# Optimization experiments

Hardware: AMD Instinct MI355X
Metric: run time of the kernel (lower is better)

## Reference

```python
import jax, jax.numpy as jnp
import numpy as np

E = 128   # embed_dim / node feature width
H = 4     # num_heads
B = 512   # number of graphs
N = 65536 # total nodes


def setup_inputs() -> dict:
    key = jax.random.key(0)
    ks = jax.random.split(key, 12)
    s = 1.0 / np.sqrt(E)
    batch = jnp.sort(jax.random.randint(ks[0], (N,), 0, B))
    return {
        "x": jax.random.normal(ks[1], (N, E), jnp.float32),
        "metal_x": jax.random.normal(ks[2], (B, E), jnp.float32),
        "batch": batch,
        "Wk": jax.random.normal(ks[3], (E, E), jnp.float32) * s,
        "bk": jnp.zeros((E,), jnp.float32),
        "Wq": jax.random.normal(ks[4], (E, E), jnp.float32) * s,
        "bq": jnp.zeros((E,), jnp.float32),
        "in_w": jax.random.normal(ks[5], (3 * E, E), jnp.float32) * s,
        "in_b": jnp.zeros((3 * E,), jnp.float32),
        "out_w": jax.random.normal(ks[6], (E, E), jnp.float32) * s,
        "out_b": jnp.zeros((E,), jnp.float32),
    }


def reference(x, metal_x, batch, Wk, bk, Wq, bq, in_w, in_b, out_w, out_b):
    n, e = x.shape
    b = metal_x.shape[0]
    nb = np.asarray(batch)
    counts_np = np.bincount(nb, minlength=b)            # nodes per graph
    L = int(counts_np.max()) + 1                        # +1 for metal token at pos 0
    counts = jnp.asarray(counts_np)
    offsets = jnp.asarray(np.concatenate([[0], np.cumsum(counts_np)[:-1]]))
    pos = jnp.arange(n) - offsets[batch] + 1            # within-graph slot (metal at 0)

    # pad_sequence: value [L, B, E], slot 0 = metal_x, slots 1.. = graph nodes
    value = jnp.zeros((L, b, e), x.dtype)
    value = value.at[pos, batch].set(x)
    value = value.at[0, jnp.arange(b)].set(metal_x)

    # FCNN key/query (single hidden linear + relu, no output head)
    k_in = jax.nn.relu(value @ Wk.T + bk)
    q_in = jax.nn.relu(value @ Wq.T + bq)

    # MultiheadAttention (batch_first=False): in_proj then per-head scaled dot-product
    hd = e // H
    q = (q_in @ in_w[:e].T + in_b[:e]).reshape(L, b, H, hd)
    k = (k_in @ in_w[e:2 * e].T + in_b[e:2 * e]).reshape(L, b, H, hd)
    v = (value @ in_w[2 * e:].T + in_b[2 * e:]).reshape(L, b, H, hd)

    scores = jnp.einsum("lbhd,mbhd->bhlm", q, k) * (hd ** -0.5)
    valid = jnp.arange(L)[None, :] < (counts + 1)[:, None]   # [B, L] key_padding mask
    scores = jnp.where(valid[:, None, None, :], scores, jnp.finfo(scores.dtype).min)
    attn = jax.nn.softmax(scores, axis=-1)
    ctx = jnp.einsum("bhlm,mbhd->lbhd", attn, v).reshape(L, b, e)
    out = ctx @ out_w.T + out_b

    x_out = out[pos, batch]      # packed node outputs [N, E]
    metal_out = out[0]           # metal token outputs [B, E]
    return x_out, metal_out
```

## Files before the change

kernel.cpp:

```cpp
#include <hip/hip_runtime.h>

#define E   128
#define HD  32
#define NB  512
#define NN  65536
#define TT  (NB + NN)
#define TE  ((size_t)TT * 128)

typedef __attribute__((ext_vector_type(8))) short short8;
typedef __attribute__((ext_vector_type(4))) float f32x4;

__device__ __forceinline__ const float* row_ptr(const float* base, const float* metal, int t) {
  return (t < NB) ? metal + (size_t)t * E : base + (size_t)(t - NB) * E;
}
__device__ __forceinline__ float* row_ptr_w(float* base, float* metal, int t) {
  return (t < NB) ? metal + (size_t)t * E : base + (size_t)(t - NB) * E;
}

__device__ __forceinline__ unsigned short f2bf_rne(float x) {
  unsigned u = __float_as_uint(x);
  return (unsigned short)((u + 0x7FFFu + ((u >> 16) & 1u)) >> 16);
}
__device__ __forceinline__ void split_bf(float x, unsigned short& h, unsigned short& l) {
  h = f2bf_rne(x);
  float hf = __uint_as_float(((unsigned)h) << 16);
  l = f2bf_rne(x - hf);
}

__global__ void k_setup(const int* __restrict__ batch, int* __restrict__ start,
                        const float* __restrict__ Wq, const float* __restrict__ Wk,
                        const float* __restrict__ in_w, const float* __restrict__ out_w,
                        unsigned short* __restrict__ Wh, unsigned short* __restrict__ Wl) {
  int b = blockIdx.x;
  if (b < 256) {
    int i = b * 256 + threadIdx.x;
    int bi = batch[i];
    int bp = (i == 0) ? -1 : batch[i - 1];
    for (int g = bp + 1; g <= bi; ++g) start[g] = i;
    if (i == NN - 1)
      for (int g = bi + 1; g <= NB; ++g) start[g] = NN;
  } else {
    int idx = (b - 256) * 256 + threadIdx.x;
    int r = idx >> 7, c = idx & 127;
    float v;
    if (r < 128)      v = Wq[r * 128 + c];
    else if (r < 256) v = Wk[(r - 128) * 128 + c];
    else if (r < 640) v = in_w[(r - 256) * 128 + c];
    else              v = out_w[(r - 640) * 128 + c];
    unsigned short h, l;
    split_bf(v, h, l);
    Wh[idx] = h;
    Wl[idx] = l;
  }
}

__global__ void k_seqmap(const int* __restrict__ batch, const int* __restrict__ start,
                         int* __restrict__ seqmap) {
  int t = blockIdx.x * 256 + threadIdx.x;
  if (t >= TT) return;
  seqmap[t] = (t < NB) ? (start[t] + t) : (t - NB + batch[t - NB] + 1);
}

__global__ __launch_bounds__(256, 2)
void k_outproj(const unsigned short* __restrict__ Ch, const unsigned short* __restrict__ Cl,
               const int* __restrict__ rowmap,
               const unsigned short* __restrict__ Wh, const unsigned short* __restrict__ Wl,
               const float* __restrict__ bias,
               float* __restrict__ Cx, float* __restrict__ Cm) {
  __shared__ char smem[40960];
  unsigned short (*AshH)[40] = (unsigned short (*)[40])smem;
  unsigned short (*AshL)[40] = (unsigned short (*)[40])(smem + 10240);
  unsigned short (*WldsH)[40] = (unsigned short (*)[40])(smem + 20480);
  unsigned short (*WldsL)[40] = (unsigned short (*)[40])(smem + 30720);

  const int tid = threadIdx.x;
  const int wave = tid >> 6;
  const int lane = tid & 63;
  const int lrow = lane & 15;
  const int q = lane >> 4;
  const int t0 = blockIdx.x * 128;

  f32x4 acc[2][8];
  #pragma unroll
  for (int mt = 0; mt < 2; ++mt)
    #pragma unroll
    for (int nt = 0; nt < 8; ++nt) acc[mt][nt] = (f32x4){0.f, 0.f, 0.f, 0.f};

  for (int ks = 0; ks < 4; ++ks) {
    __syncthreads();
    #pragma unroll
    for (int u = 0; u < 2; ++u) {
      int e = tid + u * 256;
      int row = e >> 2, seg = e & 3;
      size_t go = (size_t)rowmap[t0 + row] * 128 + ks * 32 + seg * 8;
      *(short8*)&AshH[row][seg * 8] = *(const short8*)(Ch + go);
      *(short8*)&AshL[row][seg * 8] = *(const short8*)(Cl + go);
    }
    #pragma unroll
    for (int u = 0; u < 4; ++u) {
      int idx = tid + u * 256;
      int half = idx >> 9, rem = idx & 511;
      int j = rem >> 2, seg = rem & 3;
      const unsigned short* src = (half ? Wl : Wh) + j * 128 + ks * 32 + seg * 8;
      short8 v = *(const short8*)src;
      unsigned short* dst = (half ? &WldsL[j][seg * 8] : &WldsH[j][seg * 8]);
      *(short8*)dst = v;
    }
    __syncthreads();

    short8 ah[2], al[2];
    #pragma unroll
    for (int mt = 0; mt < 2; ++mt) {
      int m = wave * 32 + mt * 16 + lrow;
      ah[mt] = *(const short8*)&AshH[m][q * 8];
      al[mt] = *(const short8*)&AshL[m][q * 8];
    }

    #pragma unroll
    for (int nt = 0; nt < 8; ++nt) {
      int j = nt * 16 + lrow;
      short8 bh = *(const short8*)&WldsH[j][q * 8];
      short8 bl = *(const short8*)&WldsL[j][q * 8];
      #pragma unroll
      for (int mt = 0; mt < 2; ++mt) {
        acc[mt][nt] = __builtin_amdgcn_mfma_f32_16x16x32_bf16(ah[mt], bh, acc[mt][nt], 0, 0, 0);
        acc[mt][nt] = __builtin_amdgcn_mfma_f32_16x16x32_bf16(al[mt], bh, acc[mt][nt], 0, 0, 0);
        acc[mt][nt] = __builtin_amdgcn_mfma_f32_16x16x32_bf16(ah[mt], bl, acc[mt][nt], 0, 0, 0);
      }
    }
  }

  #pragma unroll
  for (int mt = 0; mt < 2; ++mt) {
    #pragma unroll
    for (int reg = 0; reg < 4; ++reg) {
      int t = t0 + wave * 32 + mt * 16 + q * 4 + reg;
      float* cp = row_ptr_w(Cx, Cm, t);
      #pragma unroll
      for (int nt = 0; nt < 8; ++nt) {
        int j = nt * 16 + lrow;
        cp[j] = acc[mt][nt][reg] + bias[j];
      }
    }
  }
}

__global__ __launch_bounds__(256, 2)
void k_mega(const float* __restrict__ x, const float* __restrict__ metal_x,
            const unsigned short* __restrict__ Wh, const unsigned short* __restrict__ Wl,
            const float* __restrict__ bq, const float* __restrict__ bk,
            const float* __restrict__ in_b, float scl2,
            unsigned short* __restrict__ Voh,
            unsigned short* __restrict__ Qsh, unsigned short* __restrict__ Qsl,
            unsigned short* __restrict__ Ksh, unsigned short* __restrict__ Ksl,
            const int* __restrict__ seqmap) {
  __shared__ char smem[40960];
  float (*Afl)[36] = (float (*)[36])smem;
  unsigned short (*WldsH)[40] = (unsigned short (*)[40])(smem + 18432);
  unsigned short (*WldsL)[40] = (unsigned short (*)[40])(smem + 28672);
  unsigned short (*AshH)[40] = (unsigned short (*)[40])smem;
  unsigned short (*AshL)[40] = (unsigned short (*)[40])(smem + 10240);
  unsigned short (*W2ldsH)[40] = (unsigned short (*)[40])(smem + 20480);
  unsigned short (*W2ldsL)[40] = (unsigned short (*)[40])(smem + 30720);

  const int tid = threadIdx.x;
  const int wave = tid >> 6;
  const int lane = tid & 63;
  const int lrow = lane & 15;
  const int q = lane >> 4;
  const int group = (int)(blockIdx.x % 3);
  const int t0 = (int)(blockIdx.x / 3) * 128;

  const int w1o = (group == 0) ? 0 : (group == 1) ? 128 * 128 : 512 * 128;
  const unsigned short* W1h = Wh + w1o;
  const unsigned short* W1l = Wl + w1o;

  f32x4 acc1[2][8];
  #pragma unroll
  for (int mt = 0; mt < 2; ++mt)
    #pragma unroll
    for (int nt = 0; nt < 8; ++nt) acc1[mt][nt] = (f32x4){0.f, 0.f, 0.f, 0.f};

  for (int ks = 0; ks < 4; ++ks) {
    __syncthreads();
    #pragma unroll
    for (int u = 0; u < 4; ++u) {
      int e4 = tid + u * 256;
      int m = e4 >> 3, k4 = e4 & 7;
      const float* rp = row_ptr(x, metal_x, t0 + m);
      float4 v = ((const float4*)(rp + ks * 32))[k4];
      *(float4*)&Afl[m][k4 * 4] = v;
    }
    #pragma unroll
    for (int u = 0; u < 4; ++u) {
      int idx = tid + u * 256;
      int half = idx >> 9, rem = idx & 511;
      int j = rem >> 2, seg = rem & 3;
      const unsigned short* src = (half ? W1l : W1h) + j * 128 + ks * 32 + seg * 8;
      short8 v = *(const short8*)src;
      unsigned short* dst = (half ? &WldsL[j][seg * 8] : &WldsH[j][seg * 8]);
      *(short8*)dst = v;
    }
    __syncthreads();

    short8 ah[2], al[2];
    #pragma unroll
    for (int mt = 0; mt < 2; ++mt) {
      int m = wave * 32 + mt * 16 + lrow;
      float4 f0 = *(const float4*)&Afl[m][q * 8];
      float4 f1 = *(const float4*)&Afl[m][q * 8 + 4];
      unsigned short h, l;
      split_bf(f0.x, h, l); ah[mt][0] = (short)h; al[mt][0] = (short)l;
      split_bf(f0.y, h, l); ah[mt][1] = (short)h; al[mt][1] = (short)l;
      split_bf(f0.z, h, l); ah[mt][2] = (short)h; al[mt][2] = (short)l;
      split_bf(f0.w, h, l); ah[mt][3] = (short)h; al[mt][3] = (short)l;
      split_bf(f1.x, h, l); ah[mt][4] = (short)h; al[mt][4] = (short)l;
      split_bf(f1.y, h, l); ah[mt][5] = (short)h; al[mt][5] = (short)l;
      split_bf(f1.z, h, l); ah[mt][6] = (short)h; al[mt][6] = (short)l;
      split_bf(f1.w, h, l); ah[mt][7] = (short)h; al[mt][7] = (short)l;
    }

    #pragma unroll
    for (int nt = 0; nt < 8; ++nt) {
      int j = nt * 16 + lrow;
      short8 bh = *(const short8*)&WldsH[j][q * 8];
      short8 bl = *(const short8*)&WldsL[j][q * 8];
      #pragma unroll
      for (int mt = 0; mt < 2; ++mt) {
        acc1[mt][nt] = __builtin_amdgcn_mfma_f32_16x16x32_bf16(ah[mt], bh, acc1[mt][nt], 0, 0, 0);
        acc1[mt][nt] = __builtin_amdgcn_mfma_f32_16x16x32_bf16(al[mt], bh, acc1[mt][nt], 0, 0, 0);
        acc1[mt][nt] = __builtin_amdgcn_mfma_f32_16x16x32_bf16(ah[mt], bl, acc1[mt][nt], 0, 0, 0);
      }
    }
  }

  if (group == 2) {
    const float* bv = in_b + 2 * E;
    #pragma unroll
    for (int mt = 0; mt < 2; ++mt)
      #pragma unroll
      for (int reg = 0; reg < 4; ++reg) {
        int t = t0 + wave * 32 + mt * 16 + q * 4 + reg;
        size_t ro = (size_t)seqmap[t] * 128;
        #pragma unroll
        for (int nt = 0; nt < 8; ++nt) {
          int j = nt * 16 + lrow;
          Voh[ro + j] = f2bf_rne(acc1[mt][nt][reg] + bv[j]);
        }
      }
    return;
  }

  const int w2o = (group == 0) ? 256 * 128 : 384 * 128;
  const unsigned short* W2h = Wh + w2o;
  const unsigned short* W2l = Wl + w2o;
  const float* b1 = (group == 0) ? bq : bk;
  const float* b2 = (group == 0) ? in_b : in_b + 128;
  const float postscale = (group == 0) ? scl2 : 1.f;
  unsigned short* Oh = (group == 0) ? Qsh : Ksh;
  unsigned short* Ol = (group == 0) ? Qsl : Ksl;

  f32x4 acc2[2][8];
  #pragma unroll
  for (int mt = 0; mt < 2; ++mt)
    #pragma unroll
    for (int nt = 0; nt < 8; ++nt) acc2[mt][nt] = (f32x4){0.f, 0.f, 0.f, 0.f};

  float b1v[8];
  #pragma unroll
  for (int nt = 0; nt < 8; ++nt) b1v[nt] = b1[nt * 16 + lrow];

  #pragma unroll
  for (int ks2 = 0; ks2 < 4; ++ks2) {
    __syncthreads();
    #pragma unroll
    for (int u = 0; u < 4; ++u) {
      int idx = tid + u * 256;
      int half = idx >> 9, rem = idx & 511;
      int j = rem >> 2, seg = rem & 3;
      const unsigned short* src = (half ? W2l : W2h) + j * 128 + ks2 * 32 + seg * 8;
      short8 v = *(const short8*)src;
      unsigned short* dst = (half ? &W2ldsL[j][seg * 8] : &W2ldsH[j][seg * 8]);
      *(short8*)dst = v;
    }
    #pragma unroll
    for (int mt = 0; mt < 2; ++mt) {
      #pragma unroll
      for (int n2 = 0; n2 < 2; ++n2) {
        const int nt = ks2 * 2 + n2;
        #pragma unroll
        for (int reg = 0; reg < 4; ++reg) {
          int row = wave * 32 + mt * 16 + q * 4 + reg;
          float v = fmaxf(acc1[mt][nt][reg] + b1v[nt], 0.f);
          unsigned short h, l;
          split_bf(v, h, l);
          AshH[row][n2 * 16 + lrow] = h;
          AshL[row][n2 * 16 + lrow] = l;
        }
      }
    }
    __syncthreads();

    short8 ah[2], al[2];
    #pragma unroll
    for (int mt = 0; mt < 2; ++mt) {
      int m = wave * 32 + mt * 16 + lrow;
      ah[mt] = *(const short8*)&AshH[m][q * 8];
      al[mt] = *(const short8*)&AshL[m][q * 8];
    }
    #pragma unroll
    for (int nt = 0; nt < 8; ++nt) {
      int j = nt * 16 + lrow;
      short8 bh = *(const short8*)&W2ldsH[j][q * 8];
      short8 bl = *(const short8*)&W2ldsL[j][q * 8];
      #pragma unroll
      for (int mt = 0; mt < 2; ++mt) {
        acc2[mt][nt] = __builtin_amdgcn_mfma_f32_16x16x32_bf16(ah[mt], bh, acc2[mt][nt], 0, 0, 0);
        acc2[mt][nt] = __builtin_amdgcn_mfma_f32_16x16x32_bf16(al[mt], bh, acc2[mt][nt], 0, 0, 0);
        acc2[mt][nt] = __builtin_amdgcn_mfma_f32_16x16x32_bf16(ah[mt], bl, acc2[mt][nt], 0, 0, 0);
      }
    }
  }

  #pragma unroll
  for (int mt = 0; mt < 2; ++mt)
    #pragma unroll
    for (int reg = 0; reg < 4; ++reg) {
      int t = t0 + wave * 32 + mt * 16 + q * 4 + reg;
      size_t ro = (size_t)seqmap[t] * 128;
      #pragma unroll
      for (int nt = 0; nt < 8; ++nt) {
        int j = nt * 16 + lrow;
        float v = (acc2[mt][nt][reg] + b2[j]) * postscale;
        unsigned short h, l;
        split_bf(v, h, l);
        Oh[ro + j] = h;
        Ol[ro + j] = l;
      }
    }
}

__global__ __launch_bounds__(256, 4)
void k_flash(const unsigned short* __restrict__ Qh, const unsigned short* __restrict__ Ql,
             const unsigned short* __restrict__ Kh, const unsigned short* __restrict__ Kl,
             const unsigned short* __restrict__ Vb, const int* __restrict__ start,
             unsigned short* __restrict__ Ch, unsigned short* __restrict__ Cl) {
  __shared__ unsigned short Vlds[32][134];
  __shared__ alignas(16) unsigned PtH[4][32][20];
  __shared__ alignas(16) unsigned PtL[4][32][20];
  const int g = blockIdx.x;
  const int tid = threadIdx.x;
  const int wv = tid >> 6;
  const int lane = tid & 63;
  const int lrow = lane & 15;
  const int quad = lane >> 4;
  const int s0 = start[g];
  const int c = start[g + 1] - s0 + 1;
  const int sbase = s0 + g;
  const int hoff = wv * 32 + quad * 8;

  for (int qb = 32 * blockIdx.y; qb < c; qb += 32 * gridDim.y) {
    short8 qfh[2], qfl[2];
    #pragma unroll
    for (int mt = 0; mt < 2; ++mt) {
      int qs = qb + mt * 16 + lrow; if (qs >= c) qs = 0;
      size_t off = (size_t)(sbase + qs) * 128 + hoff;
      qfh[mt] = *(const short8*)(Qh + off);
      qfl[mt] = *(const short8*)(Ql + off);
    }
    float mr[2], lr[2];
    f32x4 O[2][2];
    #pragma unroll
    for (int mt = 0; mt < 2; ++mt) {
      mr[mt] = -3.0e38f; lr[mt] = 0.f;
      O[mt][0] = (f32x4){0.f, 0.f, 0.f, 0.f};
      O[mt][1] = (f32x4){0.f, 0.f, 0.f, 0.f};
    }

    const int nch = (c + 31) >> 5;
    for (int ch = 0; ch < nch; ++ch) {
      const int kb = ch * 32;
      short8 kfh[2], kfl[2];
      #pragma unroll
      for (int s = 0; s < 2; ++s) {
        int ks = kb + s * 16 + lrow; if (ks >= c) ks = 0;
        size_t off = (size_t)(sbase + ks) * 128 + hoff;
        kfh[s] = *(const short8*)(Kh + off);
        kfl[s] = *(const short8*)(Kl + off);
      }
      __syncthreads();
      #pragma unroll
      for (int r = 0; r < 2; ++r) {
        int key = r * 16 + (tid >> 4);
        int seg = tid & 15;
        int ks = kb + key; if (ks >= c) ks = 0;
        uint4 v = *(const uint4*)(Vb + (size_t)(sbase + ks) * 128 + seg * 8);
        unsigned* dst = (unsigned*)&Vlds[key][seg * 8];
        dst[0] = v.x; dst[1] = v.y; dst[2] = v.z; dst[3] = v.w;
      }
      __syncthreads();

      f32x4 sv[2][2];
      #pragma unroll
      for (int mt = 0; mt < 2; ++mt)
        #pragma unroll
        for (int s = 0; s < 2; ++s) {
          f32x4 z = (f32x4){0.f, 0.f, 0.f, 0.f};
          z = __builtin_amdgcn_mfma_f32_16x16x32_bf16(kfh[s], qfh[mt], z, 0, 0, 0);
          z = __builtin_amdgcn_mfma_f32_16x16x32_bf16(kfl[s], qfh[mt], z, 0, 0, 0);
          z = __builtin_amdgcn_mfma_f32_16x16x32_bf16(kfh[s], qfl[mt], z, 0, 0, 0);
          sv[mt][s] = z;
        }

      #pragma unroll
      for (int mt = 0; mt < 2; ++mt) {
        float m8 = mr[mt];
        #pragma unroll
        for (int s = 0; s < 2; ++s)
          #pragma unroll
          for (int r4 = 0; r4 < 4; ++r4) {
            bool valid = (kb + s * 16 + quad * 4 + r4) < c;
            float v = valid ? sv[mt][s][r4] : -3.0e38f;
            sv[mt][s][r4] = v;
            m8 = fmaxf(m8, v);
          }
        m8 = fmaxf(m8, __shfl_xor(m8, 16));
        m8 = fmaxf(m8, __shfl_xor(m8, 32));
        float al = exp2f(mr[mt] - m8);
        mr[mt] = m8;

        float p[2][4];
        float rs = 0.f;
        #pragma unroll
        for (int s = 0; s < 2; ++s)
          #pragma unroll
          for (int r4 = 0; r4 < 4; ++r4) {
            p[s][r4] = exp2f(sv[mt][s][r4] - m8);
            rs += p[s][r4];
          }
        rs += __shfl_xor(rs, 16);
        rs += __shfl_xor(rs, 32);
        lr[mt] = lr[mt] * al + rs;

        const int Q = mt * 16 + lrow;
        #pragma unroll
        for (int s = 0; s < 2; ++s) {
          unsigned short h0, l0, h1, l1, h2, l2, h3, l3;
          split_bf(p[s][0], h0, l0); split_bf(p[s][1], h1, l1);
          split_bf(p[s][2], h2, l2); split_bf(p[s][3], h3, l3);
          uint2 hw, lw;
          hw.x = (unsigned)h0 | ((unsigned)h1 << 16);
          hw.y = (unsigned)h2 | ((unsigned)h3 << 16);
          lw.x = (unsigned)l0 | ((unsigned)l1 << 16);
          lw.y = (unsigned)l2 | ((unsigned)l3 << 16);
          *(uint2*)&PtH[wv][Q][s * 8 + quad * 2] = hw;
          *(uint2*)&PtL[wv][Q][s * 8 + quad * 2] = lw;
        }
        #pragma unroll
        for (int nt = 0; nt < 2; ++nt)
          #pragma unroll
          for (int r4 = 0; r4 < 4; ++r4)
            O[mt][nt][r4] *= al;
      }

      short8 vf[2];
      #pragma unroll
      for (int nt = 0; nt < 2; ++nt)
        #pragma unroll
        for (int jj = 0; jj < 8; ++jj)
          vf[nt][jj] = (short)Vlds[quad * 8 + jj][wv * 32 + nt * 16 + lrow];

      #pragma unroll
      for (int mt = 0; mt < 2; ++mt) {
        short8 bh = *(const short8*)&PtH[wv][mt * 16 + lrow][quad * 4];
        short8 bl = *(const short8*)&PtL[wv][mt * 16 + lrow][quad * 4];
        #pragma unroll
        for (int nt = 0; nt < 2; ++nt) {
          O[mt][nt] = __builtin_amdgcn_mfma_f32_16x16x32_bf16(vf[nt], bh, O[mt][nt], 0, 0, 0);
          O[mt][nt] = __builtin_amdgcn_mfma_f32_16x16x32_bf16(vf[nt], bl, O[mt][nt], 0, 0, 0);
        }
      }
    }

    #pragma unroll
    for (int mt = 0; mt < 2; ++mt) {
      int qs = qb + mt * 16 + lrow;
      if (qs < c) {
        float inv = 1.f / lr[mt];
        size_t ro = (size_t)(sbase + qs) * 128 + wv * 32 + quad * 4;
        #pragma unroll
        for (int nt = 0; nt < 2; ++nt) {
          unsigned short h0, l0, h1, l1, h2, l2, h3, l3;
          split_bf(O[mt][nt][0] * inv, h0, l0);
          split_bf(O[mt][nt][1] * inv, h1, l1);
          split_bf(O[mt][nt][2] * inv, h2, l2);
          split_bf(O[mt][nt][3] * inv, h3, l3);
          uint2 hw, lw;
          hw.x = (unsigned)h0 | ((unsigned)h1 << 16);
          hw.y = (unsigned)h2 | ((unsigned)h3 << 16);
          lw.x = (unsigned)l0 | ((unsigned)l1 << 16);
          lw.y = (unsigned)l2 | ((unsigned)l3 << 16);
          *(uint2*)&Ch[ro + nt * 16] = hw;
          *(uint2*)&Cl[ro + nt * 16] = lw;
        }
      }
    }
  }
}

extern "C" void kernel_launch(void* const* d_in, const int* in_sizes, int n_in,
                              void* d_out, int out_size, void* d_ws, size_t ws_size,
                              hipStream_t stream) {
  const float* x       = (const float*)d_in[0];
  const float* metal_x = (const float*)d_in[1];
  const int*   batch   = (const int*)d_in[2];
  const float* Wk      = (const float*)d_in[3];
  const float* bk      = (const float*)d_in[4];
  const float* Wq      = (const float*)d_in[5];
  const float* bq      = (const float*)d_in[6];
  const float* in_w    = (const float*)d_in[7];
  const float* in_b    = (const float*)d_in[8];
  const float* out_w   = (const float*)d_in[9];
  const float* out_b   = (const float*)d_in[10];
  float* out = (float*)d_out;

  float* ws = (float*)d_ws;
  int* start  = (int*)d_ws;
  int* seqmap = (int*)(ws + 528);
  unsigned short* Wh = (unsigned short*)(ws + 66576);
  unsigned short* Wl = Wh + 768 * 128;
  const size_t BUF0 = 164880;
  unsigned short* Csh = (unsigned short*)(ws + BUF0);
  unsigned short* Csl = Csh + TE;
  unsigned short* Qsh = (unsigned short*)(ws + BUF0 + TE);
  unsigned short* Qsl = Qsh + TE;
  unsigned short* Ksh = (unsigned short*)(ws + BUF0 + 2 * TE);
  unsigned short* Ksl = Ksh + TE;
  unsigned short* Vsb = (unsigned short*)(ws + BUF0 + 3 * TE);

  k_setup<<<640, 256, 0, stream>>>(batch, start, Wq, Wk, in_w, out_w, Wh, Wl);
  k_seqmap<<<TT / 256, 256, 0, stream>>>(batch, start, seqmap);

  const int gb = TT / 128;
  const float SCL2 = 0.17677669529663687f * 1.4426950408889634f;

  k_mega<<<gb * 3, 256, 0, stream>>>(
      x, metal_x, Wh, Wl, bq, bk, in_b, SCL2,
      Vsb, Qsh, Qsl, Ksh, Ksl, seqmap);

  dim3 agrid(NB, 6);
  k_flash<<<agrid, 256, 0, stream>>>(Qsh, Qsl, Ksh, Ksl, Vsb, start, Csh, Csl);

  k_outproj<<<gb, 256, 0, stream>>>(
      Csh, Csl, seqmap, Wh + 640 * 128, Wl + 640 * 128,
      out_b, out, out + (size_t)NN * E);
}
```

Before: 219.7 us.

## Share staged input tile between Q and K branches in projection kernel

The projection kernel now runs one block type that computes both the Q-path and the K-path hidden layers from the same staged x tile, plus a separate block type for V. This replaces the three-way split and cuts the grid from 3x to 2x tiles, so x is loaded and split into bf16 hi/lo once instead of twice for Q and K. The cost is twice the accumulator registers, an extra weight staging pass per k-step, and uneven work between the dual and V blocks. The flash kernel also skips the key-padding mask on full key chunks.

```diff
diff --git a/kernel.cpp b/kernel.cpp
--- a/kernel.cpp
+++ b/kernel.cpp
@@ -168,18 +168,24 @@
   const int lane = tid & 63;
   const int lrow = lane & 15;
   const int q = lane >> 4;
-  const int group = (int)(blockIdx.x % 3);
-  const int t0 = (int)(blockIdx.x / 3) * 128;
-
-  const int w1o = (group == 0) ? 0 : (group == 1) ? 128 * 128 : 512 * 128;
+  const int dual = !(blockIdx.x & 1);
+  const int t0 = (int)(blockIdx.x >> 1) * 128;
+
+  const int w1o = dual ? 0 : 512 * 128;
   const unsigned short* W1h = Wh + w1o;
   const unsigned short* W1l = Wl + w1o;
-
-  f32x4 acc1[2][8];
+  const unsigned short* Wkh = Wh + 128 * 128;
+  const unsigned short* Wkl = Wl + 128 * 128;
+
+  f32x4 accQ[2][8];
+  f32x4 accK[2][8];
   #pragma unroll
   for (int mt = 0; mt < 2; ++mt)
     #pragma unroll
-    for (int nt = 0; nt < 8; ++nt) acc1[mt][nt] = (f32x4){0.f, 0.f, 0.f, 0.f};
+    for (int nt = 0; nt < 8; ++nt) {
+      accQ[mt][nt] = (f32x4){0.f, 0.f, 0.f, 0.f};
+      accK[mt][nt] = (f32x4){0.f, 0.f, 0.f, 0.f};
+    }
 
   for (int ks = 0; ks < 4; ++ks) {
     __syncthreads();
@@ -227,14 +233,41 @@
       short8 bl = *(const short8*)&WldsL[j][q * 8];
       #pragma unroll
       for (int mt = 0; mt < 2; ++mt) {
-        acc1[mt][nt] = __builtin_amdgcn_mfma_f32_16x16x32_bf16(ah[mt], bh, acc1[mt][nt], 0, 0, 0);
-        acc1[mt][nt] = __builtin_amdgcn_mfma_f32_16x16x32_bf16(al[mt], bh, acc1[mt][nt], 0, 0, 0);
-        acc1[mt][nt] = __builtin_amdgcn_mfma_f32_16x16x32_bf16(ah[mt], bl, acc1[mt][nt], 0, 0, 0);
-      }
-    }
-  }
-
-  if (group == 2) {
+        accQ[mt][nt] = __builtin_amdgcn_mfma_f32_16x16x32_bf16(ah[mt], bh, accQ[mt][nt], 0, 0, 0);
+        accQ[mt][nt] = __builtin_amdgcn_mfma_f32_16x16x32_bf16(al[mt], bh, accQ[mt][nt], 0, 0, 0);
+        accQ[mt][nt] = __builtin_amdgcn_mfma_f32_16x16x32_bf16(ah[mt], bl, accQ[mt][nt], 0, 0, 0);
+      }
+    }
+
+    if (dual) {
+      __syncthreads();
+      #pragma unroll
+      for (int u = 0; u < 4; ++u) {
+        int idx = tid + u * 256;
+        int half = idx >> 9, rem = idx & 511;
+        int j = rem >> 2, seg = rem & 3;
+        const unsigned short* src = (half ? Wkl : Wkh) + j * 128 + ks * 32 + seg * 8;
+        short8 v = *(const short8*)src;
+        unsigned short* dst = (half ? &WldsL[j][seg * 8] : &WldsH[j][seg * 8]);
+        *(short8*)dst = v;
+      }
+      __syncthreads();
+      #pragma unroll
+      for (int nt = 0; nt < 8; ++nt) {
+        int j = nt * 16 + lrow;
+        short8 ch = *(const short8*)&WldsH[j][q * 8];
+        short8 cl = *(const short8*)&WldsL[j][q * 8];
+        #pragma unroll
+        for (int mt = 0; mt < 2; ++mt) {
+          accK[mt][nt] = __builtin_amdgcn_mfma_f32_16x16x32_bf16(ah[mt], ch, accK[mt][nt], 0, 0, 0);
+          accK[mt][nt] = __builtin_amdgcn_mfma_f32_16x16x32_bf16(al[mt], ch, accK[mt][nt], 0, 0, 0);
+          accK[mt][nt] = __builtin_amdgcn_mfma_f32_16x16x32_bf16(ah[mt], cl, accK[mt][nt], 0, 0, 0);
+        }
+      }
+    }
+  }
+
+  if (!dual) {
     const float* bv = in_b + 2 * E;
     #pragma unroll
     for (int mt = 0; mt < 2; ++mt)
@@ -245,99 +278,103 @@
         #pragma unroll
         for (int nt = 0; nt < 8; ++nt) {
           int j = nt * 16 + lrow;
-          Voh[ro + j] = f2bf_rne(acc1[mt][nt][reg] + bv[j]);
+          Voh[ro + j] = f2bf_rne(accQ[mt][nt][reg] + bv[j]);
         }
       }
     return;
   }
 
-  const int w2o = (group == 0) ? 256 * 128 : 384 * 128;
-  const unsigned short* W2h = Wh + w2o;
-  const unsigned short* W2l = Wl + w2o;
-  const float* b1 = (group == 0) ? bq : bk;
-  const float* b2 = (group == 0) ? in_b : in_b + 128;
-  const float postscale = (group == 0) ? scl2 : 1.f;
-  unsigned short* Oh = (group == 0) ? Qsh : Ksh;
-  unsigned short* Ol = (group == 0) ? Qsl : Ksl;
-
-  f32x4 acc2[2][8];
   #pragma unroll
-  for (int mt = 0; mt < 2; ++mt)
-    #pragma unroll
-    for (int nt = 0; nt < 8; ++nt) acc2[mt][nt] = (f32x4){0.f, 0.f, 0.f, 0.f};
-
-  float b1v[8];
-  #pragma unroll
-  for (int nt = 0; nt < 8; ++nt) b1v[nt] = b1[nt * 16 + lrow];
-
-  #pragma unroll
-  for (int ks2 = 0; ks2 < 4; ++ks2) {
-    __syncthreads();
-    #pragma unroll
-    for (int u = 0; u < 4; ++u) {
-      int idx = tid + u * 256;
-      int half = idx >> 9, rem = idx & 511;
-      int j = rem >> 2, seg = rem & 3;
-      const unsigned short* src = (half ? W2l : W2h) + j * 128 + ks2 * 32 + seg * 8;
-      short8 v = *(const short8*)src;
-      unsigned short* dst = (half ? &W2ldsL[j][seg * 8] : &W2ldsH[j][seg * 8]);
-      *(short8*)dst = v;
-    }
-    #pragma unroll
-    for (int mt = 0; mt < 2; ++mt) {
-      #pragma unroll
-      for (int n2 = 0; n2 < 2; ++n2) {
-        const int nt = ks2 * 2 + n2;
-        #pragma unroll
-        for (int reg = 0; reg < 4; ++reg) {
-          int row = wave * 32 + mt * 16 + q * 4 + reg;
-          float v = fmaxf(acc1[mt][nt][reg] + b1v[nt], 0.f);
+  for (int pass = 0; pass < 2; ++pass) {
+    const int w2o = pass ? 384 * 128 : 256 * 128;
+    const unsigned short* W2h = Wh + w2o;
+    const unsigned short* W2l = Wl + w2o;
+    const float* b1 = pass ? bk : bq;
+    const float* b2 = pass ? in_b + 128 : in_b;
+    const float postscale = pass ? 1.f : scl2;
+    unsigned short* Oh = pass ? Ksh : Qsh;
+    unsigned short* Ol = pass ? Ksl : Qsl;
+
+    f32x4 acc2[2][8];
+    #pragma unroll
+    for (int mt = 0; mt < 2; ++mt)
+      #pragma unroll
+      for (int nt = 0; nt < 8; ++nt) acc2[mt][nt] = (f32x4){0.f, 0.f, 0.f, 0.f};
+
+    float b1v[8];
+    #pragma unroll
+    for (int nt = 0; nt < 8; ++nt) b1v[nt] = b1[nt * 16 + lrow];
+
+    #pragma unroll
+    for (int ks2 = 0; ks2 < 4; ++ks2) {
+      __syncthreads();
+      #pragma unroll
+      for (int u = 0; u < 4; ++u) {
+        int idx = tid + u * 256;
+        int half = idx >> 9, rem = idx & 511;
+        int j = rem >> 2, seg = rem & 3;
+        const unsigned short* src = (half ? W2l : W2h) + j * 128 + ks2 * 32 + seg * 8;
+        short8 v = *(const short8*)src;
+        unsigned short* dst = (half ? &W2ldsL[j][seg * 8] : &W2ldsH[j][seg * 8]);
+        *(short8*)dst = v;
+      }
+      #pragma unroll
+      for (int mt = 0; mt < 2; ++mt) {
+        #pragma unroll
+        for (int n2 = 0; n2 < 2; ++n2) {
+          const int nt = ks2 * 2 + n2;
+          #pragma unroll
+          for (int reg = 0; reg < 4; ++reg) {
+            int row = wave * 32 + mt * 16 + q * 4 + reg;
+            float hv = pass ? accK[mt][nt][reg] : accQ[mt][nt][reg];
+            float v = fmaxf(hv + b1v[nt], 0.f);
+            unsigned short h, l;
+            split_bf(v, h, l);
+            AshH[row][n2 * 16 + lrow] = h;
+            AshL[row][n2 * 16 + lrow] = l;
+          }
+        }
+      }
+      __syncthreads();
+
+      short8 ah[2], al[2];
+      #pragma unroll
+      for (int mt = 0; mt < 2; ++mt) {
+        int m = wave * 32 + mt * 16 + lrow;
+        ah[mt] = *(const short8*)&AshH[m][q * 8];
+        al[mt] = *(const short8*)&AshL[m][q * 8];
+      }
+      #pragma unroll
+      for (int nt = 0; nt < 8; ++nt) {
+        int j = nt * 16 + lrow;
+        short8 bh = *(const short8*)&W2ldsH[j][q * 8];
+        short8 bl = *(const short8*)&W2ldsL[j][q * 8];
+        #pragma unroll
+        for (int mt = 0; mt < 2; ++mt) {
+          acc2[mt][nt] = __builtin_amdgcn_mfma_f32_16x16x32_bf16(ah[mt], bh, acc2[mt][nt], 0, 0, 0);
+          acc2[mt][nt] = __builtin_amdgcn_mfma_f32_16x16x32_bf16(al[mt], bh, acc2[mt][nt], 0, 0, 0);
+          acc2[mt][nt] = __builtin_amdgcn_mfma_f32_16x16x32_bf16(ah[mt], bl, acc2[mt][nt], 0, 0, 0);
+        }
+      }
+    }
+
+    #pragma unroll
+    for (int mt = 0; mt < 2; ++mt)
+      #pragma unroll
+      for (int reg = 0; reg < 4; ++reg) {
+        int t = t0 + wave * 32 + mt * 16 + q * 4 + reg;
+        size_t ro = (size_t)seqmap[t] * 128;
+        #pragma unroll
+        for (int nt = 0; nt < 8; ++nt) {
+          int j = nt * 16 + lrow;
+          float v = (acc2[mt][nt][reg] + b2[j]) * postscale;
           unsigned short h, l;
           split_bf(v, h, l);
-          AshH[row][n2 * 16 + lrow] = h;
-          AshL[row][n2 * 16 + lrow] = l;
-        }
-      }
-    }
-    __syncthreads();
-
-    short8 ah[2], al[2];
-    #pragma unroll
-    for (int mt = 0; mt < 2; ++mt) {
-      int m = wave * 32 + mt * 16 + lrow;
-      ah[mt] = *(const short8*)&AshH[m][q * 8];
-      al[mt] = *(const short8*)&AshL[m][q * 8];
-    }
-    #pragma unroll
-    for (int nt = 0; nt < 8; ++nt) {
-      int j = nt * 16 + lrow;
-      short8 bh = *(const short8*)&W2ldsH[j][q * 8];
-      short8 bl = *(const short8*)&W2ldsL[j][q * 8];
-      #pragma unroll
-      for (int mt = 0; mt < 2; ++mt) {
-        acc2[mt][nt] = __builtin_amdgcn_mfma_f32_16x16x32_bf16(ah[mt], bh, acc2[mt][nt], 0, 0, 0);
-        acc2[mt][nt] = __builtin_amdgcn_mfma_f32_16x16x32_bf16(al[mt], bh, acc2[mt][nt], 0, 0, 0);
-        acc2[mt][nt] = __builtin_amdgcn_mfma_f32_16x16x32_bf16(ah[mt], bl, acc2[mt][nt], 0, 0, 0);
-      }
-    }
-  }
-
-  #pragma unroll
-  for (int mt = 0; mt < 2; ++mt)
-    #pragma unroll
-    for (int reg = 0; reg < 4; ++reg) {
-      int t = t0 + wave * 32 + mt * 16 + q * 4 + reg;
-      size_t ro = (size_t)seqmap[t] * 128;
-      #pragma unroll
-      for (int nt = 0; nt < 8; ++nt) {
-        int j = nt * 16 + lrow;
-        float v = (acc2[mt][nt][reg] + b2[j]) * postscale;
-        unsigned short h, l;
-        split_bf(v, h, l);
-        Oh[ro + j] = h;
-        Ol[ro + j] = l;
-      }
-    }
+          Oh[ro + j] = h;
+          Ol[ro + j] = l;
+        }
+      }
+  }
 }
 
 __global__ __launch_bounds__(256, 4)
@@ -380,6 +417,7 @@
     const int nch = (c + 31) >> 5;
     for (int ch = 0; ch < nch; ++ch) {
       const int kb = ch * 32;
+      const bool full = (kb + 32) <= c;
       short8 kfh[2], kfl[2];
       #pragma unroll
       for (int s = 0; s < 2; ++s) {
@@ -414,16 +452,19 @@
 
       #pragma unroll
       for (int mt = 0; mt < 2; ++mt) {
+        if (!full) {
+          #pragma unroll
+          for (int s = 0; s < 2; ++s)
+            #pragma unroll
+            for (int r4 = 0; r4 < 4; ++r4)
+              sv[mt][s][r4] = ((kb + s * 16 + quad * 4 + r4) < c) ? sv[mt][s][r4] : -3.0e38f;
+        }
         float m8 = mr[mt];
         #pragma unroll
         for (int s = 0; s < 2; ++s)
           #pragma unroll
-          for (int r4 = 0; r4 < 4; ++r4) {
-            bool valid = (kb + s * 16 + quad * 4 + r4) < c;
-            float v = valid ? sv[mt][s][r4] : -3.0e38f;
-            sv[mt][s][r4] = v;
-            m8 = fmaxf(m8, v);
-          }
+          for (int r4 = 0; r4 < 4; ++r4)
+            m8 = fmaxf(m8, sv[mt][s][r4]);
         m8 = fmaxf(m8, __shfl_xor(m8, 16));
         m8 = fmaxf(m8, __shfl_xor(m8, 32));
         float al = exp2f(mr[mt] - m8);
@@ -544,7 +585,7 @@
   const int gb = TT / 128;
   const float SCL2 = 0.17677669529663687f * 1.4426950408889634f;
 
-  k_mega<<<gb * 3, 256, 0, stream>>>(
+  k_mega<<<gb * 2, 256, 0, stream>>>(
       x, metal_x, Wh, Wl, bq, bk, in_b, SCL2,
       Vsb, Qsh, Qsl, Ksh, Ksl, seqmap);
 
```

After: 247.4 us. 12.6% more time.

## Stage projection epilogue through LDS for coalesced 16-byte stores; skip masking on full chunks

Applied to the files above, without the earlier changes.

The projection kernel's epilogue used to write scattered 2-byte bf16 elements straight to global memory. It now writes each wave's 16-row tile into a per-wave LDS buffer and then issues coalesced 16-byte row-segment stores to the seqmap-permuted rows, for both the V output and the split hi/lo Q/K outputs. Bias values are also hoisted into registers. Separately, the flash kernel applies key-padding masking only on the partial last chunk, which removes compare/select work from full chunks. The cost is an extra barrier and an LDS round-trip that reuses shared memory previously holding operands.

```diff
diff --git a/kernel.cpp b/kernel.cpp
--- a/kernel.cpp
+++ b/kernel.cpp
@@ -171,6 +171,9 @@
   const int group = (int)(blockIdx.x % 3);
   const int t0 = (int)(blockIdx.x / 3) * 128;
 
+  unsigned short (*EldsH)[136] = (unsigned short (*)[136])(smem + wave * 8704);
+  unsigned short (*EldsL)[136] = (unsigned short (*)[136])(smem + wave * 8704 + 4352);
+
   const int w1o = (group == 0) ? 0 : (group == 1) ? 128 * 128 : 512 * 128;
   const unsigned short* W1h = Wh + w1o;
   const unsigned short* W1l = Wl + w1o;
@@ -236,18 +239,26 @@
 
   if (group == 2) {
     const float* bv = in_b + 2 * E;
-    #pragma unroll
-    for (int mt = 0; mt < 2; ++mt)
-      #pragma unroll
-      for (int reg = 0; reg < 4; ++reg) {
-        int t = t0 + wave * 32 + mt * 16 + q * 4 + reg;
-        size_t ro = (size_t)seqmap[t] * 128;
-        #pragma unroll
-        for (int nt = 0; nt < 8; ++nt) {
-          int j = nt * 16 + lrow;
-          Voh[ro + j] = f2bf_rne(acc1[mt][nt][reg] + bv[j]);
-        }
-      }
+    float bvv[8];
+    #pragma unroll
+    for (int nt = 0; nt < 8; ++nt) bvv[nt] = bv[nt * 16 + lrow];
+    __syncthreads();
+    #pragma unroll
+    for (int mt = 0; mt < 2; ++mt) {
+      #pragma unroll
+      for (int reg = 0; reg < 4; ++reg)
+        #pragma unroll
+        for (int nt = 0; nt < 8; ++nt)
+          EldsH[q * 4 + reg][nt * 16 + lrow] = f2bf_rne(acc1[mt][nt][reg] + bvv[nt]);
+      #pragma unroll
+      for (int u = 0; u < 4; ++u) {
+        int task = lane + 64 * u;
+        int row16 = task >> 4, seg = task & 15;
+        int t = t0 + wave * 32 + mt * 16 + row16;
+        size_t ro = (size_t)seqmap[t] * 128 + seg * 8;
+        *(short8*)(Voh + ro) = *(const short8*)&EldsH[row16][seg * 8];
+      }
+    }
     return;
   }
 
@@ -322,22 +333,35 @@
     }
   }
 
-  #pragma unroll
-  for (int mt = 0; mt < 2; ++mt)
-    #pragma unroll
-    for (int reg = 0; reg < 4; ++reg) {
-      int t = t0 + wave * 32 + mt * 16 + q * 4 + reg;
-      size_t ro = (size_t)seqmap[t] * 128;
-      #pragma unroll
-      for (int nt = 0; nt < 8; ++nt) {
-        int j = nt * 16 + lrow;
-        float v = (acc2[mt][nt][reg] + b2[j]) * postscale;
-        unsigned short h, l;
-        split_bf(v, h, l);
-        Oh[ro + j] = h;
-        Ol[ro + j] = l;
-      }
-    }
+  {
+    float b2v[8];
+    #pragma unroll
+    for (int nt = 0; nt < 8; ++nt) b2v[nt] = b2[nt * 16 + lrow];
+    __syncthreads();
+    #pragma unroll
+    for (int mt = 0; mt < 2; ++mt) {
+      #pragma unroll
+      for (int reg = 0; reg < 4; ++reg)
+        #pragma unroll
+        for (int nt = 0; nt < 8; ++nt) {
+          float v = (acc2[mt][nt][reg] + b2v[nt]) * postscale;
+          unsigned short h, l;
+          split_bf(v, h, l);
+          EldsH[q * 4 + reg][nt * 16 + lrow] = h;
+          EldsL[q * 4 + reg][nt * 16 + lrow] = l;
+        }
+      #pragma unroll
+      for (int u = 0; u < 8; ++u) {
+        int task = lane + 64 * u;
+        int plane = task >> 8, row16 = (task >> 4) & 15, seg = task & 15;
+        int t = t0 + wave * 32 + mt * 16 + row16;
+        size_t ro = (size_t)seqmap[t] * 128 + seg * 8;
+        unsigned short* dst = (plane ? Ol : Oh) + ro;
+        const unsigned short* src = plane ? &EldsL[row16][seg * 8] : &EldsH[row16][seg * 8];
+        *(short8*)dst = *(const short8*)src;
+      }
+    }
+  }
 }
 
 __global__ __launch_bounds__(256, 4)
@@ -380,6 +404,7 @@
     const int nch = (c + 31) >> 5;
     for (int ch = 0; ch < nch; ++ch) {
       const int kb = ch * 32;
+      const bool full = (kb + 32) <= c;
       short8 kfh[2], kfl[2];
       #pragma unroll
       for (int s = 0; s < 2; ++s) {
@@ -414,16 +439,19 @@
 
       #pragma unroll
       for (int mt = 0; mt < 2; ++mt) {
+        if (!full) {
+          #pragma unroll
+          for (int s = 0; s < 2; ++s)
+            #pragma unroll
+            for (int r4 = 0; r4 < 4; ++r4)
+              sv[mt][s][r4] = ((kb + s * 16 + quad * 4 + r4) < c) ? sv[mt][s][r4] : -3.0e38f;
+        }
         float m8 = mr[mt];
         #pragma unroll
         for (int s = 0; s < 2; ++s)
           #pragma unroll
-          for (int r4 = 0; r4 < 4; ++r4) {
-            bool valid = (kb + s * 16 + quad * 4 + r4) < c;
-            float v = valid ? sv[mt][s][r4] : -3.0e38f;
-            sv[mt][s][r4] = v;
-            m8 = fmaxf(m8, v);
-          }
+          for (int r4 = 0; r4 < 4; ++r4)
+            m8 = fmaxf(m8, sv[mt][s][r4]);
         m8 = fmaxf(m8, __shfl_xor(m8, 16));
         m8 = fmaxf(m8, __shfl_xor(m8, 32));
         float al = exp2f(mr[mt] - m8);
```

Result: no change. 219.0 us (-0.3%).
